# Optimization experiments

Measured on AMD Instinct MI355X. Metric: run time of the kernel, lower is better.

Reference implementation:

```python
import jax, jax.numpy as jnp
import numpy as np

NEG_SLOPE = 0.2   # GATConv default leaky_relu slope
BN_EPS = 1e-5
N, D, H, DH, E, BS = 49152, 512, 8, 64, 131072, 12
N_LAYERS = 5  # conv6 exists in __init__ but is never called in forward


def setup_inputs() -> dict:
    key = jax.random.key(0)
    ks = jax.random.split(key, 12)
    s = 0.05
    x = jax.random.normal(ks[0], (N, D), jnp.float32)
    edge_index = jax.random.randint(ks[1], (2, E), 0, N, jnp.int64)
    Ws = jax.random.normal(ks[2], (N_LAYERS, D, H * DH), jnp.float32) * s
    Asrc = jax.random.normal(ks[3], (N_LAYERS, H, DH), jnp.float32) * s
    Adst = jax.random.normal(ks[4], (N_LAYERS, H, DH), jnp.float32) * s
    Bconv = jax.random.normal(ks[5], (N_LAYERS, H * DH), jnp.float32) * s
    Gamma = jnp.ones((N_LAYERS, D), jnp.float32)
    Beta = jnp.zeros((N_LAYERS, D), jnp.float32)
    Wl = jax.random.normal(ks[6], (D, 1), jnp.float32) * s
    bl = jnp.zeros((1,), jnp.float32)
    return {"x": x, "edge_index": edge_index, "Ws": Ws, "Asrc": Asrc,
            "Adst": Adst, "Bconv": Bconv, "Gamma": Gamma, "Beta": Beta,
            "Wl": Wl, "bl": bl, "bs": BS}


def _gat_conv(x, src, dst, W, a_src, a_dst, b):
    n = x.shape[0]
    h = (x @ W).reshape(n, H, DH)                      # [N,H,DH]
    al_s = jnp.einsum('nhd,hd->nh', h, a_src)          # [N,H]
    al_d = jnp.einsum('nhd,hd->nh', h, a_dst)
    e = jax.nn.leaky_relu(al_s[src] + al_d[dst], NEG_SLOPE)  # [Etot,H]
    # segment softmax over incoming edges of each dst node
    m = jax.ops.segment_max(e, dst, num_segments=n)
    p = jnp.exp(e - m[dst])
    z = jax.ops.segment_sum(p, dst, num_segments=n)
    alpha = p / (z[dst] + 1e-16)
    out = jax.ops.segment_sum(alpha[:, :, None] * h[src], dst, num_segments=n)
    return out.reshape(n, H * DH) + b


def _batch_norm(x, gamma, beta):
    mu = x.mean(0)
    var = x.var(0)  # biased, as torch BN uses for normalization
    return (x - mu) * jax.lax.rsqrt(var + BN_EPS) * gamma + beta


def reference(x, edge_index, Ws, Asrc, Adst, Bconv, Gamma, Beta, Wl, bl, bs):
    n = x.shape[0]
    loops = jnp.arange(n, dtype=edge_index.dtype)      # add_self_loops=True
    src = jnp.concatenate([edge_index[0], loops])
    dst = jnp.concatenate([edge_index[1], loops])
    for i in range(N_LAYERS):
        x = _gat_conv(x, src, dst, Ws[i], Asrc[i], Adst[i], Bconv[i])
        x = jax.nn.relu(_batch_norm(x, Gamma[i], Beta[i]))
    w = x @ Wl + bl                                    # [N,1]
    return w.reshape(bs, -1)
```

## Files before the change

kernel.cpp:

```cpp
#include <hip/hip_runtime.h>
#include <cstdint>

#define N_NODES 49152
#define DIM 512
#define NH 8
#define DHEAD 64
#define NE 131072
#define ETOT (NE + N_NODES)
#define NLAYERS 5
#define AGG_NODES 32
#define AGG_BLOCKS (N_NODES / AGG_NODES)

typedef short short8 __attribute__((ext_vector_type(8)));
typedef float floatx4 __attribute__((ext_vector_type(4)));

__device__ __forceinline__ float bf2f(unsigned short v) {
  union { unsigned int u; float f; } x; x.u = ((unsigned int)v) << 16; return x.f;
}
__device__ __forceinline__ unsigned short f2bf(float f) {
  union { float f; unsigned int u; } x; x.f = f;
  unsigned int r = x.u + 0x7fffu + ((x.u >> 16) & 1u);
  return (unsigned short)(r >> 16);
}
__device__ __forceinline__ void async_load16(const void* g, void* l) {
  __builtin_amdgcn_global_load_lds((const __attribute__((address_space(1))) void*)g,
                                   (__attribute__((address_space(3))) void*)l, 16, 0, 0);
}

__global__ void transpose_w_r18(const float* __restrict__ Ws, unsigned short* __restrict__ WT)
{
  __shared__ float tile[32][33];
  const int l  = blockIdx.z;
  const int nt = blockIdx.x * 32, kt = blockIdx.y * 32;
  const int tx = threadIdx.x & 31, ty = threadIdx.x >> 5;
  #pragma unroll
  for (int r = 0; r < 32; r += 8)
    tile[ty + r][tx] = Ws[(size_t)l*DIM*DIM + (size_t)(kt + ty + r)*DIM + nt + tx];
  __syncthreads();
  #pragma unroll
  for (int r = 0; r < 32; r += 8)
    WT[(size_t)l*DIM*DIM + (size_t)(nt + ty + r)*DIM + kt + tx] = f2bf(tile[tx][ty + r]);
}

__global__ void repack_edges_r18(const int* __restrict__ raw, int* __restrict__ eidx)
{
  const int i = blockIdx.x * 256 + threadIdx.x;
  bool is64 = true;
  #pragma unroll
  for (int j = 0; j < 16; j++) is64 = is64 && (raw[2*j + 1] == 0);
  int v;
  if (is64) v = (int)((const long long*)raw)[i];
  else      v = raw[i];
  eidx[i] = v;
}

__global__ void init_counts_r18(int* __restrict__ counts) {
  counts[blockIdx.x * 256 + threadIdx.x] = 1;
}
__global__ void hist_dst_r18(const int* __restrict__ eidx, int* __restrict__ counts) {
  const int i = blockIdx.x * 256 + threadIdx.x;
  atomicAdd(&counts[eidx[NE + i]], 1);
}
__global__ void scan_kernel_r18(const int* __restrict__ counts, int* __restrict__ offs, int* __restrict__ cursor)
{
  __shared__ int tot[1024];
  const int t = threadIdx.x;
  const int base = t * 48;
  int s = 0;
  for (int i = 0; i < 48; i++) s += counts[base + i];
  tot[t] = s;
  __syncthreads();
  for (int o = 1; o < 1024; o <<= 1) {
    int v = (t >= o) ? tot[t - o] : 0;
    __syncthreads();
    tot[t] += v;
    __syncthreads();
  }
  int run = tot[t] - s;
  for (int i = 0; i < 48; i++) {
    offs[base + i] = run;
    cursor[base + i] = run;
    run += counts[base + i];
  }
  if (t == 1023) offs[N_NODES] = tot[1023];
}
__global__ void scatter_edges_r18(const int* __restrict__ eidx, int* __restrict__ cursor, int* __restrict__ csrc)
{
  const int i = blockIdx.x * 256 + threadIdx.x;
  int s, d;
  if (i < NE) { s = eidx[i]; d = eidx[NE + i]; }
  else        { s = i - NE; d = s; }
  const int pos = atomicAdd(&cursor[d], 1);
  csrc[pos] = s;
}

__global__ __launch_bounds__(512, 4) void gemm_bt_r18(const float* __restrict__ Af,
                                                      const unsigned short* __restrict__ Ab,
                                                      const unsigned short* __restrict__ BT,
                                                      const float* __restrict__ asrc,
                                                      const float* __restrict__ adst,
                                                      const float* __restrict__ bnscale,
                                                      const float* __restrict__ bnshift,
                                                      unsigned short* __restrict__ C,
                                                      float* __restrict__ als,
                                                      float* __restrict__ ald)
{
  __shared__ unsigned short As[128 * 64];
  __shared__ unsigned short Bs[256 * 64];
  const int d = blockIdx.x;
  const int m_blk = (d & 7) * 48 + ((d >> 3) >> 1);
  const int n_blk = (d >> 3) & 1;
  const int m0 = m_blk * 128;
  const int n0 = n_blk * 256;
  const int tid = threadIdx.x;
  const int wv = tid >> 6, lane = tid & 63;
  const int wr = (wv & 1) * 64, wc = (wv >> 1) * 64;
  const int q = lane >> 4, c16 = lane & 15;
  const int arow = lane >> 3;
  const int acol = (((lane & 7) ^ arow) * 8);
  const int sr = tid >> 3;
  const int sk = (tid & 7) * 8;
  const int swk = (((tid & 7) ^ (sr & 7)) * 8);
  const int rx = (c16 & 7);
  const bool isconv = (Af != nullptr);

  floatx4 acc[4][4] = {};

  for (int k0 = 0; k0 < DIM; k0 += 64) {
    #pragma unroll
    for (int t = 0; t < 4; t++) {
      const int cb = wv * 4 + t;
      async_load16(BT + (size_t)(n0 + cb*8 + arow)*DIM + k0 + acol, &Bs[cb * 512]);
    }
    if (isconv) {
      #pragma unroll
      for (int t = 0; t < 2; t++) {
        const float4 v0 = *(const float4*)&Af[(size_t)(m0 + sr + t*64) * DIM + k0 + sk];
        const float4 v1 = *(const float4*)&Af[(size_t)(m0 + sr + t*64) * DIM + k0 + sk + 4];
        const float v[8] = {v0.x, v0.y, v0.z, v0.w, v1.x, v1.y, v1.z, v1.w};
        unsigned int ov[4];
        #pragma unroll
        for (int j = 0; j < 4; j++)
          ov[j] = (unsigned int)f2bf(v[2*j]) | ((unsigned int)f2bf(v[2*j+1]) << 16);
        *(uint4*)&As[(sr + t*64) * 64 + swk] = *(const uint4*)ov;
      }
    } else if (bnscale) {
      const uint4 x0 = *(const uint4*)&Ab[(size_t)(m0 + sr)      * DIM + k0 + sk];
      const uint4 x1 = *(const uint4*)&Ab[(size_t)(m0 + sr + 64) * DIM + k0 + sk];
      const float4 sc0 = *(const float4*)&bnscale[k0 + sk];
      const float4 sc1 = *(const float4*)&bnscale[k0 + sk + 4];
      const float4 sh0 = *(const float4*)&bnshift[k0 + sk];
      const float4 sh1 = *(const float4*)&bnshift[k0 + sk + 4];
      const float scv[8] = {sc0.x, sc0.y, sc0.z, sc0.w, sc1.x, sc1.y, sc1.z, sc1.w};
      const float shv[8] = {sh0.x, sh0.y, sh0.z, sh0.w, sh1.x, sh1.y, sh1.z, sh1.w};
      const uint4 xs[2] = {x0, x1};
      #pragma unroll
      for (int t = 0; t < 2; t++) {
        const unsigned int* xp = (const unsigned int*)&xs[t];
        unsigned int ov[4];
        #pragma unroll
        for (int j = 0; j < 4; j++) {
          const float a = bf2f((unsigned short)(xp[j] & 0xffffu));
          const float b = bf2f((unsigned short)(xp[j] >> 16));
          const float ya = fmaxf(0.f, a * scv[2*j]     + shv[2*j]);
          const float yb = fmaxf(0.f, b * scv[2*j + 1] + shv[2*j + 1]);
          ov[j] = (unsigned int)f2bf(ya) | ((unsigned int)f2bf(yb) << 16);
        }
        *(uint4*)&As[(sr + t*64) * 64 + swk] = *(const uint4*)ov;
      }
    } else {
      #pragma unroll
      for (int t = 0; t < 2; t++) {
        const int cb = wv * 2 + t;
        async_load16(Ab + (size_t)(m0 + cb*8 + arow)*DIM + k0 + acol, &As[cb * 512]);
      }
    }
    __syncthreads();
    #pragma unroll
    for (int kk = 0; kk < 64; kk += 32) {
      const int cg = (kk >> 3) + q;
      const int po = ((cg ^ rx) * 8);
      short8 aF[4], bF[4];
      #pragma unroll
      for (int mt = 0; mt < 4; mt++)
        aF[mt] = *(const short8*)&As[(wr + mt*16 + c16) * 64 + po];
      #pragma unroll
      for (int nt = 0; nt < 4; nt++)
        bF[nt] = *(const short8*)&Bs[(wc + nt*16 + c16) * 64 + po];
      #pragma unroll
      for (int mt = 0; mt < 4; mt++)
        #pragma unroll
        for (int nt = 0; nt < 4; nt++)
          acc[mt][nt] = __builtin_amdgcn_mfma_f32_16x16x32_bf16(aF[mt], bF[nt], acc[mt][nt], 0, 0, 0);
    }
    __syncthreads();
  }
  #pragma unroll
  for (int mt = 0; mt < 4; mt++) {
    #pragma unroll
    for (int nt = 0; nt < 4; nt++) {
      const int col = n0 + wc + nt*16 + c16;
      #pragma unroll
      for (int r = 0; r < 4; r++) {
        const int row = m0 + wr + mt*16 + q*4 + r;
        C[(size_t)row * DIM + col] = f2bf(acc[mt][nt][r]);
      }
    }
  }
  const int head = 4 * n_blk + (wc >> 6);
  float as_[4], ad_[4];
  #pragma unroll
  for (int nt = 0; nt < 4; nt++) {
    const int d2 = nt * 16 + c16;
    as_[nt] = asrc[head * DHEAD + d2];
    ad_[nt] = adst[head * DHEAD + d2];
  }
  #pragma unroll
  for (int mt = 0; mt < 4; mt++) {
    #pragma unroll
    for (int r = 0; r < 4; r++) {
      float ss = 0.f, sd = 0.f;
      #pragma unroll
      for (int nt = 0; nt < 4; nt++) {
        ss += acc[mt][nt][r] * as_[nt];
        sd += acc[mt][nt][r] * ad_[nt];
      }
      #pragma unroll
      for (int msk = 1; msk <= 8; msk <<= 1) {
        ss += __shfl_xor(ss, msk, 64);
        sd += __shfl_xor(sd, msk, 64);
      }
      if (c16 == 0) {
        const int row = m0 + wr + mt*16 + q*4 + r;
        als[row * NH + head] = ss;
        ald[row * NH + head] = sd;
      }
    }
  }
}

__global__ __launch_bounds__(512, 4) void gat_agg_r18(const unsigned short* __restrict__ Hm,
    const float* __restrict__ als, const float* __restrict__ ald,
    const int* __restrict__ offs, const int* __restrict__ csrc,
    const float* __restrict__ bconv, unsigned short* __restrict__ Xout,
    float* __restrict__ ps, float* __restrict__ pq)
{
  __shared__ float red[8][1024];
  const int wv = threadIdx.x >> 6, lane = threadIdx.x & 63;
  const int hd = lane >> 3;
  const int hp = lane & 7;
  const int slot = lane >> 3;
  const float4 bA = ((const float4*)(bconv + (size_t)lane * 8))[0];
  const float4 bB = ((const float4*)(bconv + (size_t)lane * 8))[1];
  const float barr[8] = {bA.x, bA.y, bA.z, bA.w, bB.x, bB.y, bB.z, bB.w};
  float cs[8] = {}, cq[8] = {};

  #pragma unroll 1
  for (int i = 0; i < 4; i++) {
    const int node = blockIdx.x * AGG_NODES + wv * 4 + i;
    const int e0 = offs[node], e1 = offs[node + 1];
    const int deg = e1 - e0;
    float acc[8] = {};
    float zinv;

    if (deg <= 8) {
      const float aldp = ald[node * NH + hp];
      const int myS = csrc[e0 + ((lane < deg) ? lane : 0)];
      const int s_slot = __shfl(myS, slot, 64);
      float lg = als[s_slot * NH + hp] + aldp;
      lg = lg > 0.f ? lg : 0.2f * lg;
      const float lgv = (slot < deg) ? lg : -1e30f;
      float mx = fmaxf(lgv, __shfl_xor(lgv, 8, 64));
      mx = fmaxf(mx, __shfl_xor(mx, 16, 64));
      mx = fmaxf(mx, __shfl_xor(mx, 32, 64));
      const float w = __expf(lgv - mx);
      float z = w + __shfl_xor(w, 8, 64);
      z += __shfl_xor(z, 16, 64);
      z += __shfl_xor(z, 32, 64);
      zinv = 1.f / (__shfl(z, hd, 64) + 1e-16f);

      #pragma unroll
      for (int g = 0; g < 2; g++) {
        const int b = g * 4;
        if (b < deg) {
          const int k1 = (b+1 < deg) ? b+1 : 0;
          const int k2 = (b+2 < deg) ? b+2 : 0;
          const int k3 = (b+3 < deg) ? b+3 : 0;
          const int s0 = __shfl(myS, b,  64);
          const int s1 = __shfl(myS, k1, 64);
          const int s2 = __shfl(myS, k2, 64);
          const int s3 = __shfl(myS, k3, 64);
          const uint4 h0v = *(const uint4*)&Hm[(size_t)s0 * DIM + lane * 8];
          const uint4 h1v = *(const uint4*)&Hm[(size_t)s1 * DIM + lane * 8];
          const uint4 h2v = *(const uint4*)&Hm[(size_t)s2 * DIM + lane * 8];
          const uint4 h3v = *(const uint4*)&Hm[(size_t)s3 * DIM + lane * 8];
          const float w0 = __shfl(w, (b+0)*8 + hd, 64);
          const float w1 = __shfl(w, (b+1)*8 + hd, 64);
          const float w2 = __shfl(w, (b+2)*8 + hd, 64);
          const float w3 = __shfl(w, (b+3)*8 + hd, 64);
          const unsigned int* p0 = (const unsigned int*)&h0v;
          const unsigned int* p1 = (const unsigned int*)&h1v;
          const unsigned int* p2 = (const unsigned int*)&h2v;
          const unsigned int* p3 = (const unsigned int*)&h3v;
          #pragma unroll
          for (int j = 0; j < 4; j++) {
            acc[2*j]   += w0 * bf2f((unsigned short)(p0[j] & 0xffffu))
                        + w1 * bf2f((unsigned short)(p1[j] & 0xffffu))
                        + w2 * bf2f((unsigned short)(p2[j] & 0xffffu))
                        + w3 * bf2f((unsigned short)(p3[j] & 0xffffu));
            acc[2*j+1] += w0 * bf2f((unsigned short)(p0[j] >> 16))
                        + w1 * bf2f((unsigned short)(p1[j] >> 16))
                        + w2 * bf2f((unsigned short)(p2[j] >> 16))
                        + w3 * bf2f((unsigned short)(p3[j] >> 16));
          }
        }
      }
    } else if (deg <= 64) {
      const float aldp = ald[node * NH + hp];
      const int myS = (lane < deg) ? csrc[e0 + lane] : 0;
      const int nr = (deg + 7) >> 3;
      float lgsto[8];
      #pragma unroll
      for (int r = 0; r < 8; r++) {
        if (r < nr) {
          const int k = r * 8 + slot;
          const int s = __shfl(myS, k & 63, 64);
          float lg = als[s * NH + hp] + aldp;
          lg = lg > 0.f ? lg : 0.2f * lg;
          lgsto[r] = (k < deg) ? lg : -1e30f;
        } else lgsto[r] = -1e30f;
      }
      float m = lgsto[0];
      #pragma unroll
      for (int r = 1; r < 8; r++) m = fmaxf(m, lgsto[r]);
      m = fmaxf(m, __shfl_xor(m, 8, 64));
      m = fmaxf(m, __shfl_xor(m, 16, 64));
      m = fmaxf(m, __shfl_xor(m, 32, 64));
      float z = 0.f;
      float wsto[8];
      #pragma unroll
      for (int r = 0; r < 8; r++) {
        if (r < nr) {
          const float w = __expf(lgsto[r] - m);
          wsto[r] = w; z += w;
        } else wsto[r] = 0.f;
      }
      z += __shfl_xor(z, 8, 64);
      z += __shfl_xor(z, 16, 64);
      z += __shfl_xor(z, 32, 64);
      zinv = 1.f / (__shfl(z, hd, 64) + 1e-16f);

      int sn = __shfl(myS, 0, 64);
      uint4 hv = *(const uint4*)&Hm[(size_t)sn * DIM + lane * 8];
      #pragma unroll
      for (int r = 0; r < 8; r++) {
        if (r * 8 < deg) {
          const int kmax = (deg - r * 8 < 8) ? (deg - r * 8) : 8;
          for (int kk = 0; kk < kmax; kk++) {
            const uint4 hcur = hv;
            const int k = r * 8 + kk;
            if (k + 1 < deg) {
              const int s2 = __shfl(myS, (k + 1) & 63, 64);
              hv = *(const uint4*)&Hm[(size_t)s2 * DIM + lane * 8];
            }
            const float w = __shfl(wsto[r], (kk << 3) + hd, 64);
            const unsigned int* hpx = (const unsigned int*)&hcur;
            #pragma unroll
            for (int j = 0; j < 4; j++) {
              acc[2*j]   += w * bf2f((unsigned short)(hpx[j] & 0xffffu));
              acc[2*j+1] += w * bf2f((unsigned short)(hpx[j] >> 16));
            }
          }
        }
      }
    } else {
      const float aldv = ald[node * NH + hd];
      float m = -1e30f, z = 0.f;
      for (int e = e0; e < e1; e++) {
        const int s = csrc[e];
        float lg = als[s * NH + hd] + aldv;
        lg = lg > 0.f ? lg : 0.2f * lg;
        const float mn = fmaxf(m, lg);
        const float sf = __expf(m - mn);
        const float w  = __expf(lg - mn);
        z = z * sf + w;
        const uint4 hv = *(const uint4*)&Hm[(size_t)s * DIM + lane * 8];
        const unsigned int* hpx = (const unsigned int*)&hv;
        #pragma unroll
        for (int j = 0; j < 4; j++) {
          acc[2*j]   = acc[2*j]   * sf + w * bf2f((unsigned short)(hpx[j] & 0xffffu));
          acc[2*j+1] = acc[2*j+1] * sf + w * bf2f((unsigned short)(hpx[j] >> 16));
        }
        m = mn;
      }
      zinv = 1.f / (z + 1e-16f);
    }

    unsigned int ov[4];
    #pragma unroll
    for (int j = 0; j < 4; j++) {
      const unsigned short b0 = f2bf(acc[2*j] * zinv + barr[2*j]);
      const unsigned short b1 = f2bf(acc[2*j+1] * zinv + barr[2*j+1]);
      ov[j] = (unsigned int)b0 | ((unsigned int)b1 << 16);
      const float y0 = bf2f(b0), y1 = bf2f(b1);
      cs[2*j]   += y0; cq[2*j]   += y0 * y0;
      cs[2*j+1] += y1; cq[2*j+1] += y1 * y1;
    }
    *(uint4*)&Xout[(size_t)node * DIM + lane * 8] = *(const uint4*)ov;
  }
  #pragma unroll
  for (int j = 0; j < 8; j++) {
    red[wv][lane * 8 + j] = cs[j];
    red[wv][512 + lane * 8 + j] = cq[j];
  }
  __syncthreads();
  const int t = threadIdx.x;
  float s = 0.f, q = 0.f;
  #pragma unroll
  for (int w = 0; w < 8; w++) {
    s += red[w][t];
    q += red[w][512 + t];
  }
  ps[(size_t)blockIdx.x * 512 + t] = s;
  pq[(size_t)blockIdx.x * 512 + t] = q;
}

__global__ __launch_bounds__(256) void bn_reduce_r18(const float* __restrict__ ps, const float* __restrict__ pq,
                                                     const float* __restrict__ gamma, const float* __restrict__ beta,
                                                     float* __restrict__ scale, float* __restrict__ shift)
{
  __shared__ float rs[256], rq[256];
  const int c = blockIdx.x;
  const int t = threadIdx.x;
  float s = 0.f, q = 0.f;
  for (int b = t; b < AGG_BLOCKS; b += 256) {
    s += ps[(size_t)b * 512 + c];
    q += pq[(size_t)b * 512 + c];
  }
  rs[t] = s; rq[t] = q;
  __syncthreads();
  for (int o = 128; o > 0; o >>= 1) {
    if (t < o) { rs[t] += rs[t + o]; rq[t] += rq[t + o]; }
    __syncthreads();
  }
  if (t == 0) {
    const float inv = 1.0f / (float)N_NODES;
    const float mean = rs[0] * inv;
    float var = rq[0] * inv - mean * mean;
    var = fmaxf(var, 0.f);
    const float rsq = rsqrtf(var + 1e-5f);
    const float sc = gamma[c] * rsq;
    scale[c] = sc;
    shift[c] = beta[c] - mean * sc;
  }
}

__global__ __launch_bounds__(256) void final_head_r18(const unsigned short* __restrict__ X,
    const float* __restrict__ scale, const float* __restrict__ shift,
    const float* __restrict__ wl, const float* __restrict__ blp,
    float* __restrict__ out)
{
  const int wv = threadIdx.x >> 6, lane = threadIdx.x & 63;
  const int node = blockIdx.x * 4 + wv;
  const uint4 xv = *(const uint4*)&X[(size_t)node * DIM + lane * 8];
  const unsigned int* xp = (const unsigned int*)&xv;
  const int c0 = lane * 8;
  float s = 0.f;
  #pragma unroll
  for (int i = 0; i < 4; i++) {
    const float a0 = bf2f((unsigned short)(xp[i] & 0xffffu));
    const float a1 = bf2f((unsigned short)(xp[i] >> 16));
    const float y0 = fmaxf(0.f, a0 * scale[c0 + 2*i]     + shift[c0 + 2*i]);
    const float y1 = fmaxf(0.f, a1 * scale[c0 + 2*i + 1] + shift[c0 + 2*i + 1]);
    s += y0 * wl[c0 + 2*i] + y1 * wl[c0 + 2*i + 1];
  }
  #pragma unroll
  for (int msk = 32; msk >= 1; msk >>= 1) s += __shfl_xor(s, msk, 64);
  if (lane == 0) out[node] = s + blp[0];
}

extern "C" void kernel_launch(void* const* d_in, const int* in_sizes, int n_in,
                              void* d_out, int out_size, void* d_ws, size_t ws_size,
                              hipStream_t stream)
{
  const float* x_in  = (const float*)d_in[0];
  const int*   ei    = (const int*)d_in[1];
  const float* Ws    = (const float*)d_in[2];
  const float* Asrc  = (const float*)d_in[3];
  const float* Adst  = (const float*)d_in[4];
  const float* Bconv = (const float*)d_in[5];
  const float* Gamma = (const float*)d_in[6];
  const float* Beta  = (const float*)d_in[7];
  const float* Wl    = (const float*)d_in[8];
  const float* bl    = (const float*)d_in[9];
  float* out = (float*)d_out;

  char* ws = (char*)d_ws;
  size_t off = 0;
  auto alloc = [&](size_t b) { char* p = ws + off; off += (b + 255) & ~(size_t)255; return p; };
  unsigned short* xbuf = (unsigned short*)alloc((size_t)N_NODES * DIM * 2);
  unsigned short* hbuf = (unsigned short*)alloc((size_t)N_NODES * DIM * 2);
  unsigned short* WT   = (unsigned short*)alloc((size_t)NLAYERS * DIM * DIM * 2);
  float* als   = (float*)alloc((size_t)N_NODES * NH * 4);
  float* ald   = (float*)alloc((size_t)N_NODES * NH * 4);
  int* eidx    = (int*)alloc((size_t)2 * NE * 4);
  int* counts  = (int*)alloc((size_t)N_NODES * 4);
  int* offs    = (int*)alloc(((size_t)N_NODES + 1) * 4);
  int* cursor  = (int*)alloc((size_t)N_NODES * 4);
  int* csrc    = (int*)alloc((size_t)ETOT * 4);
  float* ps    = (float*)alloc((size_t)AGG_BLOCKS * 512 * 4);
  float* pq    = (float*)alloc((size_t)AGG_BLOCKS * 512 * 4);
  float* scale = (float*)alloc(512 * 4);
  float* shift = (float*)alloc(512 * 4);

  transpose_w_r18<<<dim3(16, 16, 5), 256, 0, stream>>>(Ws, WT);
  repack_edges_r18<<<(2 * NE) / 256, 256, 0, stream>>>(ei, eidx);
  init_counts_r18<<<N_NODES / 256, 256, 0, stream>>>(counts);
  hist_dst_r18<<<NE / 256, 256, 0, stream>>>(eidx, counts);
  scan_kernel_r18<<<1, 1024, 0, stream>>>(counts, offs, cursor);
  scatter_edges_r18<<<ETOT / 256, 256, 0, stream>>>(eidx, cursor, csrc);

  for (int l = 0; l < NLAYERS; l++) {
    gemm_bt_r18<<<768, 512, 0, stream>>>(
        (l == 0) ? x_in : nullptr, (l == 0) ? nullptr : xbuf,
        WT + (size_t)l * DIM * DIM,
        Asrc + l * NH * DHEAD, Adst + l * NH * DHEAD,
        (l == 0) ? nullptr : scale, (l == 0) ? nullptr : shift,
        hbuf, als, ald);
    gat_agg_r18<<<AGG_BLOCKS, 512, 0, stream>>>(hbuf, als, ald, offs, csrc,
                                                Bconv + l * DIM, xbuf, ps, pq);
    bn_reduce_r18<<<512, 256, 0, stream>>>(ps, pq, Gamma + l * DIM, Beta + l * DIM, scale, shift);
  }
  final_head_r18<<<N_NODES / 4, 256, 0, stream>>>(xbuf, scale, shift, Wl, bl, out);
}
```

Baseline: 726.8 us.

## Software-pipeline GEMM K-loop with double-buffered B tiles and register-prefetched A

The GEMM main loop now issues global loads for the next K-tile (A into registers, B async into a second LDS buffer) before running the MFMAs on the current tile. A is then converted and written to LDS after a barrier, so memory latency overlaps with compute. The previous fully-async bf16 A path is replaced by a register path for every non-conv layer. LDS use grows by another 32 KB for the second B buffer, which may lower occupancy below the requested 4 blocks, and register pressure rises.

```diff
diff --git a/kernel.cpp b/kernel.cpp
--- a/kernel.cpp
+++ b/kernel.cpp
@@ -27,7 +27,7 @@
                                    (__attribute__((address_space(3))) void*)l, 16, 0, 0);
 }
 
-__global__ void transpose_w_r18(const float* __restrict__ Ws, unsigned short* __restrict__ WT)
+__global__ void transpose_w_r19(const float* __restrict__ Ws, unsigned short* __restrict__ WT)
 {
   __shared__ float tile[32][33];
   const int l  = blockIdx.z;
@@ -42,7 +42,7 @@
     WT[(size_t)l*DIM*DIM + (size_t)(nt + ty + r)*DIM + kt + tx] = f2bf(tile[tx][ty + r]);
 }
 
-__global__ void repack_edges_r18(const int* __restrict__ raw, int* __restrict__ eidx)
+__global__ void repack_edges_r19(const int* __restrict__ raw, int* __restrict__ eidx)
 {
   const int i = blockIdx.x * 256 + threadIdx.x;
   bool is64 = true;
@@ -54,14 +54,14 @@
   eidx[i] = v;
 }
 
-__global__ void init_counts_r18(int* __restrict__ counts) {
+__global__ void init_counts_r19(int* __restrict__ counts) {
   counts[blockIdx.x * 256 + threadIdx.x] = 1;
 }
-__global__ void hist_dst_r18(const int* __restrict__ eidx, int* __restrict__ counts) {
+__global__ void hist_dst_r19(const int* __restrict__ eidx, int* __restrict__ counts) {
   const int i = blockIdx.x * 256 + threadIdx.x;
   atomicAdd(&counts[eidx[NE + i]], 1);
 }
-__global__ void scan_kernel_r18(const int* __restrict__ counts, int* __restrict__ offs, int* __restrict__ cursor)
+__global__ void scan_kernel_r19(const int* __restrict__ counts, int* __restrict__ offs, int* __restrict__ cursor)
 {
   __shared__ int tot[1024];
   const int t = threadIdx.x;
@@ -84,7 +84,7 @@
   }
   if (t == 1023) offs[N_NODES] = tot[1023];
 }
-__global__ void scatter_edges_r18(const int* __restrict__ eidx, int* __restrict__ cursor, int* __restrict__ csrc)
+__global__ void scatter_edges_r19(const int* __restrict__ eidx, int* __restrict__ cursor, int* __restrict__ csrc)
 {
   const int i = blockIdx.x * 256 + threadIdx.x;
   int s, d;
@@ -94,7 +94,7 @@
   csrc[pos] = s;
 }
 
-__global__ __launch_bounds__(512, 4) void gemm_bt_r18(const float* __restrict__ Af,
+__global__ __launch_bounds__(512, 4) void gemm_bt_r19(const float* __restrict__ Af,
                                                       const unsigned short* __restrict__ Ab,
                                                       const unsigned short* __restrict__ BT,
                                                       const float* __restrict__ asrc,
@@ -106,7 +106,7 @@
                                                       float* __restrict__ ald)
 {
   __shared__ unsigned short As[128 * 64];
-  __shared__ unsigned short Bs[256 * 64];
+  __shared__ unsigned short Bs[2][256 * 64];
   const int d = blockIdx.x;
   const int m_blk = (d & 7) * 48 + ((d >> 3) >> 1);
   const int n_blk = (d >> 3) & 1;
@@ -125,57 +125,78 @@
   const bool isconv = (Af != nullptr);
 
   floatx4 acc[4][4] = {};
-
-  for (int k0 = 0; k0 < DIM; k0 += 64) {
-    #pragma unroll
-    for (int t = 0; t < 4; t++) {
-      const int cb = wv * 4 + t;
-      async_load16(BT + (size_t)(n0 + cb*8 + arow)*DIM + k0 + acol, &Bs[cb * 512]);
-    }
-    if (isconv) {
-      #pragma unroll
-      for (int t = 0; t < 2; t++) {
-        const float4 v0 = *(const float4*)&Af[(size_t)(m0 + sr + t*64) * DIM + k0 + sk];
-        const float4 v1 = *(const float4*)&Af[(size_t)(m0 + sr + t*64) * DIM + k0 + sk + 4];
-        const float v[8] = {v0.x, v0.y, v0.z, v0.w, v1.x, v1.y, v1.z, v1.w};
-        unsigned int ov[4];
-        #pragma unroll
-        for (int j = 0; j < 4; j++)
-          ov[j] = (unsigned int)f2bf(v[2*j]) | ((unsigned int)f2bf(v[2*j+1]) << 16);
-        *(uint4*)&As[(sr + t*64) * 64 + swk] = *(const uint4*)ov;
-      }
-    } else if (bnscale) {
-      const uint4 x0 = *(const uint4*)&Ab[(size_t)(m0 + sr)      * DIM + k0 + sk];
-      const uint4 x1 = *(const uint4*)&Ab[(size_t)(m0 + sr + 64) * DIM + k0 + sk];
-      const float4 sc0 = *(const float4*)&bnscale[k0 + sk];
-      const float4 sc1 = *(const float4*)&bnscale[k0 + sk + 4];
-      const float4 sh0 = *(const float4*)&bnshift[k0 + sk];
-      const float4 sh1 = *(const float4*)&bnshift[k0 + sk + 4];
-      const float scv[8] = {sc0.x, sc0.y, sc0.z, sc0.w, sc1.x, sc1.y, sc1.z, sc1.w};
-      const float shv[8] = {sh0.x, sh0.y, sh0.z, sh0.w, sh1.x, sh1.y, sh1.z, sh1.w};
-      const uint4 xs[2] = {x0, x1};
-      #pragma unroll
-      for (int t = 0; t < 2; t++) {
-        const unsigned int* xp = (const unsigned int*)&xs[t];
-        unsigned int ov[4];
-        #pragma unroll
-        for (int j = 0; j < 4; j++) {
-          const float a = bf2f((unsigned short)(xp[j] & 0xffffu));
-          const float b = bf2f((unsigned short)(xp[j] >> 16));
-          const float ya = fmaxf(0.f, a * scv[2*j]     + shv[2*j]);
-          const float yb = fmaxf(0.f, b * scv[2*j + 1] + shv[2*j + 1]);
-          ov[j] = (unsigned int)f2bf(ya) | ((unsigned int)f2bf(yb) << 16);
-        }
-        *(uint4*)&As[(sr + t*64) * 64 + swk] = *(const uint4*)ov;
-      }
-    } else {
-      #pragma unroll
-      for (int t = 0; t < 2; t++) {
-        const int cb = wv * 2 + t;
-        async_load16(Ab + (size_t)(m0 + cb*8 + arow)*DIM + k0 + acol, &As[cb * 512]);
-      }
-    }
-    __syncthreads();
+  float4 pf0a, pf0b, pf1a, pf1b;
+  uint4  pb0, pb1;
+  float4 psc0, psc1, psh0, psh1;
+
+#define ISSUE_A(K) do { \
+    if (isconv) { \
+      pf0a = *(const float4*)&Af[(size_t)(m0 + sr) * DIM + (K) + sk]; \
+      pf0b = *(const float4*)&Af[(size_t)(m0 + sr) * DIM + (K) + sk + 4]; \
+      pf1a = *(const float4*)&Af[(size_t)(m0 + sr + 64) * DIM + (K) + sk]; \
+      pf1b = *(const float4*)&Af[(size_t)(m0 + sr + 64) * DIM + (K) + sk + 4]; \
+    } else { \
+      pb0 = *(const uint4*)&Ab[(size_t)(m0 + sr) * DIM + (K) + sk]; \
+      pb1 = *(const uint4*)&Ab[(size_t)(m0 + sr + 64) * DIM + (K) + sk]; \
+      psc0 = *(const float4*)&bnscale[(K) + sk];  psc1 = *(const float4*)&bnscale[(K) + sk + 4]; \
+      psh0 = *(const float4*)&bnshift[(K) + sk];  psh1 = *(const float4*)&bnshift[(K) + sk + 4]; \
+    } } while (0)
+
+#define ISSUE_B(K, BUF) do { \
+    _Pragma("unroll") \
+    for (int t_ = 0; t_ < 4; t_++) { \
+      const int cb_ = wv * 4 + t_; \
+      async_load16(BT + (size_t)(n0 + cb_*8 + arow)*DIM + (K) + acol, &Bs[BUF][cb_ * 512]); \
+    } } while (0)
+
+#define WRITE_A() do { \
+    unsigned int ov0[4], ov1[4]; \
+    if (isconv) { \
+      const float v0[8] = {pf0a.x,pf0a.y,pf0a.z,pf0a.w,pf0b.x,pf0b.y,pf0b.z,pf0b.w}; \
+      const float v1[8] = {pf1a.x,pf1a.y,pf1a.z,pf1a.w,pf1b.x,pf1b.y,pf1b.z,pf1b.w}; \
+      _Pragma("unroll") \
+      for (int j = 0; j < 4; j++) { \
+        ov0[j] = (unsigned int)f2bf(v0[2*j]) | ((unsigned int)f2bf(v0[2*j+1]) << 16); \
+        ov1[j] = (unsigned int)f2bf(v1[2*j]) | ((unsigned int)f2bf(v1[2*j+1]) << 16); \
+      } \
+    } else { \
+      const float scv[8] = {psc0.x,psc0.y,psc0.z,psc0.w,psc1.x,psc1.y,psc1.z,psc1.w}; \
+      const float shv[8] = {psh0.x,psh0.y,psh0.z,psh0.w,psh1.x,psh1.y,psh1.z,psh1.w}; \
+      const unsigned int* xp0 = (const unsigned int*)&pb0; \
+      const unsigned int* xp1 = (const unsigned int*)&pb1; \
+      _Pragma("unroll") \
+      for (int j = 0; j < 4; j++) { \
+        const float a0 = bf2f((unsigned short)(xp0[j] & 0xffffu)); \
+        const float b0 = bf2f((unsigned short)(xp0[j] >> 16)); \
+        const float a1 = bf2f((unsigned short)(xp1[j] & 0xffffu)); \
+        const float b1 = bf2f((unsigned short)(xp1[j] >> 16)); \
+        const float y0a = fmaxf(0.f, a0 * scv[2*j]     + shv[2*j]); \
+        const float y0b = fmaxf(0.f, b0 * scv[2*j + 1] + shv[2*j + 1]); \
+        const float y1a = fmaxf(0.f, a1 * scv[2*j]     + shv[2*j]); \
+        const float y1b = fmaxf(0.f, b1 * scv[2*j + 1] + shv[2*j + 1]); \
+        ov0[j] = (unsigned int)f2bf(y0a) | ((unsigned int)f2bf(y0b) << 16); \
+        ov1[j] = (unsigned int)f2bf(y1a) | ((unsigned int)f2bf(y1b) << 16); \
+      } \
+    } \
+    *(uint4*)&As[sr * 64 + swk]        = *(const uint4*)ov0; \
+    *(uint4*)&As[(sr + 64) * 64 + swk] = *(const uint4*)ov1; \
+  } while (0)
+
+  ISSUE_A(0);
+  ISSUE_B(0, 0);
+  WRITE_A();
+  asm volatile("s_waitcnt vmcnt(0) lgkmcnt(0)" ::: "memory");
+  __builtin_amdgcn_sched_barrier(0);
+  asm volatile("s_barrier" ::: "memory");
+
+  #pragma unroll
+  for (int t = 0; t < 8; ++t) {
+    const int k0 = t * 64;
+    const int cur = t & 1;
+    if (t < 7) {
+      ISSUE_A(k0 + 64);
+      ISSUE_B(k0 + 64, cur ^ 1);
+    }
     #pragma unroll
     for (int kk = 0; kk < 64; kk += 32) {
       const int cg = (kk >> 3) + q;
@@ -186,15 +207,27 @@
         aF[mt] = *(const short8*)&As[(wr + mt*16 + c16) * 64 + po];
       #pragma unroll
       for (int nt = 0; nt < 4; nt++)
-        bF[nt] = *(const short8*)&Bs[(wc + nt*16 + c16) * 64 + po];
+        bF[nt] = *(const short8*)&Bs[cur][(wc + nt*16 + c16) * 64 + po];
       #pragma unroll
       for (int mt = 0; mt < 4; mt++)
         #pragma unroll
         for (int nt = 0; nt < 4; nt++)
           acc[mt][nt] = __builtin_amdgcn_mfma_f32_16x16x32_bf16(aF[mt], bF[nt], acc[mt][nt], 0, 0, 0);
     }
-    __syncthreads();
-  }
+    if (t < 7) {
+      asm volatile("s_waitcnt lgkmcnt(0)" ::: "memory");
+      __builtin_amdgcn_sched_barrier(0);
+      asm volatile("s_barrier" ::: "memory");
+      WRITE_A();
+      asm volatile("s_waitcnt vmcnt(0) lgkmcnt(0)" ::: "memory");
+      __builtin_amdgcn_sched_barrier(0);
+      asm volatile("s_barrier" ::: "memory");
+    }
+  }
+#undef ISSUE_A
+#undef ISSUE_B
+#undef WRITE_A
+
   #pragma unroll
   for (int mt = 0; mt < 4; mt++) {
     #pragma unroll
@@ -239,7 +272,7 @@
   }
 }
 
-__global__ __launch_bounds__(512, 4) void gat_agg_r18(const unsigned short* __restrict__ Hm,
+__global__ __launch_bounds__(512, 4) void gat_agg_r19(const unsigned short* __restrict__ Hm,
     const float* __restrict__ als, const float* __restrict__ ald,
     const int* __restrict__ offs, const int* __restrict__ csrc,
     const float* __restrict__ bconv, unsigned short* __restrict__ Xout,
@@ -425,7 +458,7 @@
   pq[(size_t)blockIdx.x * 512 + t] = q;
 }
 
-__global__ __launch_bounds__(256) void bn_reduce_r18(const float* __restrict__ ps, const float* __restrict__ pq,
+__global__ __launch_bounds__(256) void bn_reduce_r19(const float* __restrict__ ps, const float* __restrict__ pq,
                                                      const float* __restrict__ gamma, const float* __restrict__ beta,
                                                      float* __restrict__ scale, float* __restrict__ shift)
 {
@@ -455,7 +488,7 @@
   }
 }
 
-__global__ __launch_bounds__(256) void final_head_r18(const unsigned short* __restrict__ X,
+__global__ __launch_bounds__(256) void final_head_r19(const unsigned short* __restrict__ X,
     const float* __restrict__ scale, const float* __restrict__ shift,
     const float* __restrict__ wl, const float* __restrict__ blp,
     float* __restrict__ out)
@@ -513,23 +546,23 @@
   float* scale = (float*)alloc(512 * 4);
   float* shift = (float*)alloc(512 * 4);
 
-  transpose_w_r18<<<dim3(16, 16, 5), 256, 0, stream>>>(Ws, WT);
-  repack_edges_r18<<<(2 * NE) / 256, 256, 0, stream>>>(ei, eidx);
-  init_counts_r18<<<N_NODES / 256, 256, 0, stream>>>(counts);
-  hist_dst_r18<<<NE / 256, 256, 0, stream>>>(eidx, counts);
-  scan_kernel_r18<<<1, 1024, 0, stream>>>(counts, offs, cursor);
-  scatter_edges_r18<<<ETOT / 256, 256, 0, stream>>>(eidx, cursor, csrc);
+  transpose_w_r19<<<dim3(16, 16, 5), 256, 0, stream>>>(Ws, WT);
+  repack_edges_r19<<<(2 * NE) / 256, 256, 0, stream>>>(ei, eidx);
+  init_counts_r19<<<N_NODES / 256, 256, 0, stream>>>(counts);
+  hist_dst_r19<<<NE / 256, 256, 0, stream>>>(eidx, counts);
+  scan_kernel_r19<<<1, 1024, 0, stream>>>(counts, offs, cursor);
+  scatter_edges_r19<<<ETOT / 256, 256, 0, stream>>>(eidx, cursor, csrc);
 
   for (int l = 0; l < NLAYERS; l++) {
-    gemm_bt_r18<<<768, 512, 0, stream>>>(
+    gemm_bt_r19<<<768, 512, 0, stream>>>(
         (l == 0) ? x_in : nullptr, (l == 0) ? nullptr : xbuf,
         WT + (size_t)l * DIM * DIM,
         Asrc + l * NH * DHEAD, Adst + l * NH * DHEAD,
         (l == 0) ? nullptr : scale, (l == 0) ? nullptr : shift,
         hbuf, als, ald);
-    gat_agg_r18<<<AGG_BLOCKS, 512, 0, stream>>>(hbuf, als, ald, offs, csrc,
+    gat_agg_r19<<<AGG_BLOCKS, 512, 0, stream>>>(hbuf, als, ald, offs, csrc,
                                                 Bconv + l * DIM, xbuf, ps, pq);
-    bn_reduce_r18<<<512, 256, 0, stream>>>(ps, pq, Gamma + l * DIM, Beta + l * DIM, scale, shift);
-  }
-  final_head_r18<<<N_NODES / 4, 256, 0, stream>>>(xbuf, scale, shift, Wl, bl, out);
-}
+    bn_reduce_r19<<<512, 256, 0, stream>>>(ps, pq, Gamma + l * DIM, Beta + l * DIM, scale, shift);
+  }
+  final_head_r19<<<N_NODES / 4, 256, 0, stream>>>(xbuf, scale, shift, Wl, bl, out);
+}
```

Measured after the change: 1.380 ms. 1.9x slower.
